# Kernel tuning notes

Hardware: AMD Instinct MI355X
Metric: run time of the kernel (lower is better)

## Reference

```python
import jax, jax.numpy as jnp
import numpy as np

B, N, K = 64, 128, 12
D_ATOM, D_NBR, D_NEW = 256, 320, 256
H, DK = 8, 32  # D_NEW = H * DK
LN_EPS = 1e-5
NEG_INF = -1e9


def setup_inputs() -> dict:
    key = jax.random.key(0)
    ks = jax.random.split(key, 10)
    atom_feature = jax.random.normal(ks[0], (B, N, D_ATOM), jnp.float32)
    atom_neighbor_feature = jax.random.normal(ks[1], (B, N, K, D_NBR), jnp.float32)
    # valid-neighbor masks from random neighbor counts in [1, K]
    counts = jax.random.randint(ks[2], (B, N), 1, K + 1)
    valid = (jnp.arange(K)[None, None, :] < counts[:, :, None]).astype(jnp.float32)
    atom_attend_mask = valid[..., None]                      # (B,N,K,1), 1=real neighbor
    atom_softmax_mask = (1.0 - valid[..., None]) * NEG_INF   # (B,N,K,1), additive
    # parameters
    s = 1.0 / np.sqrt(D_ATOM)
    W_atom = jax.random.uniform(ks[3], (D_ATOM, D_NEW), jnp.float32, -s, s)
    b_atom = jnp.zeros((D_NEW,), jnp.float32)
    s2 = 1.0 / np.sqrt(D_NBR)
    W_nbr = jax.random.uniform(ks[4], (D_NBR, D_NEW), jnp.float32, -s2, s2)
    b_nbr = jnp.zeros((D_NEW,), jnp.float32)
    s3 = 1.0 / np.sqrt(DK)
    w_align = jax.random.uniform(ks[5], (DK, 1), jnp.float32, -s3, s3)
    b_align = jnp.zeros((1,), jnp.float32)
    ln_gamma = jnp.ones((D_NEW,), jnp.float32)
    ln_beta = jnp.zeros((D_NEW,), jnp.float32)
    return dict(atom_feature=atom_feature, atom_neighbor_feature=atom_neighbor_feature,
                atom_softmax_mask=atom_softmax_mask, atom_attend_mask=atom_attend_mask,
                W_atom=W_atom, b_atom=b_atom, W_nbr=W_nbr, b_nbr=b_nbr,
                w_align=w_align, b_align=b_align, ln_gamma=ln_gamma, ln_beta=ln_beta)


def reference(atom_feature, atom_neighbor_feature, atom_softmax_mask, atom_attend_mask,
              W_atom, b_atom, W_nbr, b_nbr, w_align, b_align, ln_gamma, ln_beta):
    # dropout is identity at eval time
    h = atom_feature @ W_atom + b_atom                    # (B,N,D_NEW)
    e = atom_neighbor_feature @ W_nbr + b_nbr             # (B,N,K,D_NEW)
    h = h.reshape(B, N, 1, H, DK)                         # broadcast over K
    e = e.reshape(B, N, K, H, DK)
    # GATv2: act(h_i + e_j) then per-head linear score
    feat = jax.nn.leaky_relu(h + e)                       # slope 0.01 == torch default
    score = feat @ w_align + b_align                      # (B,N,K,H,1)
    score = score + atom_softmax_mask[:, :, :, None, :]   # additive -inf on pad
    attn = jax.nn.softmax(score, axis=2)                  # softmax over neighbors K
    attn = attn * atom_attend_mask[:, :, :, None, :]
    ctx = jnp.sum(attn * e, axis=2).reshape(B, N, H * DK)  # (B,N,D_NEW)
    # LayerNorm
    mu = jnp.mean(ctx, axis=-1, keepdims=True)
    xc = ctx - mu
    var = jnp.mean(xc * xc, axis=-1, keepdims=True)
    return xc * jax.lax.rsqrt(var + LN_EPS) * ln_gamma + ln_beta
```

## Files before the change

kernel.cpp:

```cpp
#include <hip/hip_runtime.h>

#define KN 12
#define DNBR 320
#define DNEW 256
#define BN_TOT 8192
#define ATB 2
#define NKS_E 10
#define NKS_H 8
#define ASTR_E 328
#define ASTR_H 264
#define H_OFF 294912

typedef short bf8_t __attribute__((ext_vector_type(8)));
typedef float f32x4 __attribute__((ext_vector_type(4)));
typedef unsigned short us8 __attribute__((ext_vector_type(8)));
using u16 = unsigned short;
using u32 = unsigned int;

__device__ __forceinline__ u16 f2bf(float f) {
    u32 x = __float_as_uint(f);
    return (u16)((x + 0x7fffu + ((x >> 16) & 1u)) >> 16);
}

__device__ __forceinline__ us8 pack8(float4 a, float4 b) {
    us8 v;
    v[0] = f2bf(a.x); v[1] = f2bf(a.y); v[2] = f2bf(a.z); v[3] = f2bf(a.w);
    v[4] = f2bf(b.x); v[5] = f2bf(b.y); v[6] = f2bf(b.z); v[7] = f2bf(b.w);
    return v;
}

__global__ __launch_bounds__(256) void build_b2(
    const float* __restrict__ Wn, const float* __restrict__ Wa,
    u16* __restrict__ B2)
{
    int tile = blockIdx.x * 4 + (threadIdx.x >> 6);
    int l = threadIdx.x & 63;
    int q = l >> 4, m = l & 15;
    us8 v;
    if (tile < 160) {
        int ks = tile >> 4, nt = tile & 15;
        int col = nt * 16 + m;
#pragma unroll
        for (int e = 0; e < 8; e++)
            v[e] = f2bf(Wn[(ks * 32 + q * 8 + e) * DNEW + col]);
    } else {
        int tt = tile - 160;
        int ks = tt >> 4, nt = tt & 15;
        int col = nt * 16 + m;
#pragma unroll
        for (int e = 0; e < 8; e++)
            v[e] = f2bf(Wa[(ks * 32 + q * 8 + e) * DNEW + col]);
    }
    *(us8*)&B2[(size_t)tile * 512 + l * 8] = v;
}

__global__ __launch_bounds__(256) void h_pre(
    const float* __restrict__ atomf, const u16* __restrict__ B2,
    const float* __restrict__ ba, float* __restrict__ h_g)
{
    __shared__ u16 A[32 * ASTR_H];

    const int t = threadIdx.x;
    const int l = t & 63, w = t >> 6, q = l >> 4, m = l & 15;
    const int ab = blockIdx.x * 32;

    const float* base = atomf + (size_t)ab * DNEW;
    for (int i = t; i < 1024; i += 256) {
        float4 v0 = *(const float4*)(base + i * 8);
        float4 v1 = *(const float4*)(base + i * 8 + 4);
        int a = i >> 5, c8 = i & 31;
        *(us8*)&A[a * ASTR_H + c8 * 8] = pack8(v0, v1);
    }
    __syncthreads();

    f32x4 acc[2][4];
#pragma unroll
    for (int mt = 0; mt < 2; mt++)
#pragma unroll
        for (int j = 0; j < 4; j++) acc[mt][j] = (f32x4){0.f, 0.f, 0.f, 0.f};

    for (int ks = 0; ks < NKS_H; ks++) {
        bf8_t af0 = *(bf8_t*)&A[m * ASTR_H + ks * 32 + q * 8];
        bf8_t af1 = *(bf8_t*)&A[(16 + m) * ASTR_H + ks * 32 + q * 8];
#pragma unroll
        for (int j = 0; j < 4; j++) {
            bf8_t bfj = *(const bf8_t*)&B2[((size_t)(160 + ks * 16 + w * 4 + j) * 64 + l) * 8];
            acc[0][j] = __builtin_amdgcn_mfma_f32_16x16x32_bf16(af0, bfj, acc[0][j], 0, 0, 0);
            acc[1][j] = __builtin_amdgcn_mfma_f32_16x16x32_bf16(af1, bfj, acc[1][j], 0, 0, 0);
        }
    }
#pragma unroll
    for (int mt = 0; mt < 2; mt++)
#pragma unroll
        for (int j = 0; j < 4; j++) {
            int col = w * 64 + j * 16 + m;
            float bav = ba[col];
#pragma unroll
            for (int r = 0; r < 4; r++) {
                int row = ab + mt * 16 + q * 4 + r;
                h_g[(size_t)row * DNEW + col] = acc[mt][j][r] + bav;
            }
        }
}

__global__ __launch_bounds__(256, 6) void fused_all(
    const float* __restrict__ nbrf,
    const float* __restrict__ smaskg, const float* __restrict__ amaskg,
    const u16* __restrict__ B2, const float* __restrict__ h_g,
    const float* __restrict__ bnb, const float* __restrict__ walg,
    const float* __restrict__ balg, const float* __restrict__ gam,
    const float* __restrict__ bet, float* __restrict__ out)
{
    __shared__ u16 A_e[28 * ASTR_E];
    __shared__ float bnb_l[256];
    __shared__ float wal_l[32];
    __shared__ float smask_l[ATB * KN];
    __shared__ float amask_l[ATB * KN];
    __shared__ float red_l[ATB][8];

    const int t = threadIdx.x;
    const int l = t & 63, w = t >> 6, q = l >> 4, m = l & 15;
    const int a0 = blockIdx.x * ATB;

    bnb_l[t] = bnb[t];
    if (t < 32) wal_l[t] = walg[t];
    else if (t >= 32 && t < 32 + ATB * KN)
        smask_l[t - 32] = smaskg[(size_t)a0 * KN + (t - 32)] + balg[0];
    else if (t >= 64 && t < 64 + ATB * KN)
        amask_l[t - 64] = amaskg[(size_t)a0 * KN + (t - 64)];

    const float* nbase = nbrf + (size_t)a0 * (KN * DNBR);
    for (int i = t; i < 960; i += 256) {
        float4 v0 = *(const float4*)(nbase + i * 8);
        float4 v1 = *(const float4*)(nbase + i * 8 + 4);
        int at = i / 480, rem = i - at * 480;
        int row = rem / 40, c8 = rem - row * 40;
        *(us8*)&A_e[(at * 12 + row) * ASTR_E + c8 * 8] = pack8(v0, v1);
    }
    if (t < 164) {
        int rr = t / 41, c8 = t - rr * 41;
        us8 z = {0, 0, 0, 0, 0, 0, 0, 0};
        *(us8*)&A_e[(24 + rr) * ASTR_E + c8 * 8] = z;
    }

    float hv[ATB][4];
#pragma unroll
    for (int j = 0; j < 4; j++) {
        int col = w * 64 + j * 16 + m;
        hv[0][j] = h_g[(size_t)(a0 + 0) * DNEW + col];
        hv[1][j] = h_g[(size_t)(a0 + 1) * DNEW + col];
    }

    __syncthreads();

    f32x4 acc_e[ATB][4];
#pragma unroll
    for (int at = 0; at < ATB; at++)
#pragma unroll
        for (int j = 0; j < 4; j++) acc_e[at][j] = (f32x4){0.f, 0.f, 0.f, 0.f};

    for (int ks = 0; ks < NKS_E; ks++) {
        bf8_t af0 = *(bf8_t*)&A_e[m * ASTR_E + ks * 32 + q * 8];
        bf8_t af1 = *(bf8_t*)&A_e[(12 + m) * ASTR_E + ks * 32 + q * 8];
#pragma unroll
        for (int j = 0; j < 4; j++) {
            bf8_t bfj = *(const bf8_t*)&B2[((size_t)(ks * 16 + w * 4 + j) * 64 + l) * 8];
            acc_e[0][j] = __builtin_amdgcn_mfma_f32_16x16x32_bf16(af0, bfj, acc_e[0][j], 0, 0, 0);
            acc_e[1][j] = __builtin_amdgcn_mfma_f32_16x16x32_bf16(af1, bfj, acc_e[1][j], 0, 0, 0);
        }
    }

#pragma unroll
    for (int j = 0; j < 4; j++) {
        float bv = bnb_l[w * 64 + j * 16 + m];
#pragma unroll
        for (int at = 0; at < ATB; at++)
#pragma unroll
            for (int r = 0; r < 4; r++) acc_e[at][j][r] += bv;
    }

    float wv[4];
#pragma unroll
    for (int j = 0; j < 4; j++) wv[j] = wal_l[(j * 16 + m) & 31];

    float ctxv[ATB][4];
#pragma unroll
    for (int at = 0; at < ATB; at++) {
        float s1 = 0.f, s2 = 0.f;
#pragma unroll
        for (int jj = 0; jj < 2; jj++) {
            float p[4];
#pragma unroll
            for (int r = 0; r < 4; r++) {
                float pp = 0.f;
#pragma unroll
                for (int jo = 0; jo < 2; jo++) {
                    int j = jj * 2 + jo;
                    float f = acc_e[at][j][r] + hv[at][j];
                    f = f > 0.f ? f : 0.01f * f;
                    pp = fmaf(f, wv[j], pp);
                }
                pp += __shfl_xor(pp, 1);
                pp += __shfl_xor(pp, 2);
                pp += __shfl_xor(pp, 4);
                pp += __shfl_xor(pp, 8);
                p[r] = (q < 3) ? pp + smask_l[at * KN + q * 4 + r] : -1e30f;
            }
            float mx = fmaxf(fmaxf(p[0], p[1]), fmaxf(p[2], p[3]));
            mx = fmaxf(mx, __shfl_xor(mx, 16));
            mx = fmaxf(mx, __shfl_xor(mx, 32));
            float ex[4], ss = 0.f;
#pragma unroll
            for (int r = 0; r < 4; r++) {
                ex[r] = (q < 3) ? __expf(p[r] - mx) : 0.f;
                ss += ex[r];
            }
            ss += __shfl_xor(ss, 16);
            ss += __shfl_xor(ss, 32);
            float inv = 1.f / ss;
            float am[4];
#pragma unroll
            for (int r = 0; r < 4; r++)
                am[r] = (q < 3) ? ex[r] * inv * amask_l[at * KN + q * 4 + r] : 0.f;
#pragma unroll
            for (int jo = 0; jo < 2; jo++) {
                int j = jj * 2 + jo;
                float cp = am[0] * acc_e[at][j][0] + am[1] * acc_e[at][j][1] +
                           am[2] * acc_e[at][j][2] + am[3] * acc_e[at][j][3];
                cp += __shfl_xor(cp, 16);
                cp += __shfl_xor(cp, 32);
                ctxv[at][j] = cp;
                s1 += cp;
                s2 += cp * cp;
            }
        }
#pragma unroll
        for (int off = 1; off < 16; off <<= 1) {
            s1 += __shfl_xor(s1, off);
            s2 += __shfl_xor(s2, off);
        }
        if (l == 0) { red_l[at][w] = s1; red_l[at][4 + w] = s2; }
    }
    __syncthreads();

#pragma unroll
    for (int at = 0; at < ATB; at++) {
        float ts1 = red_l[at][0] + red_l[at][1] + red_l[at][2] + red_l[at][3];
        float ts2 = red_l[at][4] + red_l[at][5] + red_l[at][6] + red_l[at][7];
        float mu = ts1 * (1.f / 256.f);
        float var = ts2 * (1.f / 256.f) - mu * mu;
        var = fmaxf(var, 0.f);
        float rs = rsqrtf(var + 1e-5f);
        if (q == 0) {
#pragma unroll
            for (int j = 0; j < 4; j++) {
                int col = w * 64 + j * 16 + m;
                out[(size_t)(a0 + at) * DNEW + col] =
                    (ctxv[at][j] - mu) * rs * gam[col] + bet[col];
            }
        }
    }
}

extern "C" void kernel_launch(void* const* d_in, const int* in_sizes, int n_in,
                              void* d_out, int out_size, void* d_ws, size_t ws_size,
                              hipStream_t stream) {
    const float* atomf = (const float*)d_in[0];
    const float* nbrf  = (const float*)d_in[1];
    const float* smask = (const float*)d_in[2];
    const float* amask = (const float*)d_in[3];
    const float* Wa    = (const float*)d_in[4];
    const float* ba    = (const float*)d_in[5];
    const float* Wn    = (const float*)d_in[6];
    const float* bnb   = (const float*)d_in[7];
    const float* wal   = (const float*)d_in[8];
    const float* bal   = (const float*)d_in[9];
    const float* gam   = (const float*)d_in[10];
    const float* bet   = (const float*)d_in[11];
    float* outp = (float*)d_out;

    u16* B2 = (u16*)d_ws;
    float* h_g = (float*)((char*)d_ws + H_OFF);

    build_b2<<<72, 256, 0, stream>>>(Wn, Wa, B2);
    h_pre<<<BN_TOT / 32, 256, 0, stream>>>(atomf, B2, ba, h_g);
    fused_all<<<BN_TOT / ATB, 256, 0, stream>>>(nbrf, smask, amask, B2, h_g,
                                                bnb, wal, bal, gam, bet, outp);
}
```

Baseline: 265.3 us.

## Load neighbor features directly into MFMA A-fragments, dropping LDS staging

The neighbor-feature tile no longer goes through shared memory. Each lane now loads its own fp32 neighbor row slice from global memory and converts it to bf16 in registers with v_cvt_pk_bf16_f32. Bias, align weights and masks are read straight into registers, which removes the LDS buffer and the __syncthreads. Each of the four waves in a block now reloads the same A data from global memory (leaning on the cache), and the occupancy hint drops from 6 to 4 blocks to leave more register room.

Result: slower. 289.2 us (+9.0%).

```diff
diff --git a/kernel.cpp b/kernel.cpp
--- a/kernel.cpp
+++ b/kernel.cpp
@@ -7,7 +7,6 @@
 #define ATB 2
 #define NKS_E 10
 #define NKS_H 8
-#define ASTR_E 328
 #define ASTR_H 264
 #define H_OFF 294912
 
@@ -27,6 +26,17 @@
     v[0] = f2bf(a.x); v[1] = f2bf(a.y); v[2] = f2bf(a.z); v[3] = f2bf(a.w);
     v[4] = f2bf(b.x); v[5] = f2bf(b.y); v[6] = f2bf(b.z); v[7] = f2bf(b.w);
     return v;
+}
+
+__device__ __forceinline__ bf8_t cvt8(float4 a, float4 b) {
+    u32 r0, r1, r2, r3;
+    asm("v_cvt_pk_bf16_f32 %0, %1, %2" : "=v"(r0) : "v"(a.x), "v"(a.y));
+    asm("v_cvt_pk_bf16_f32 %0, %1, %2" : "=v"(r1) : "v"(a.z), "v"(a.w));
+    asm("v_cvt_pk_bf16_f32 %0, %1, %2" : "=v"(r2) : "v"(b.x), "v"(b.y));
+    asm("v_cvt_pk_bf16_f32 %0, %1, %2" : "=v"(r3) : "v"(b.z), "v"(b.w));
+    union { u32 u[4]; bf8_t v; } cv;
+    cv.u[0] = r0; cv.u[1] = r1; cv.u[2] = r2; cv.u[3] = r3;
+    return cv.v;
 }
 
 __global__ __launch_bounds__(256) void build_b2(
@@ -103,7 +113,7 @@
         }
 }
 
-__global__ __launch_bounds__(256, 6) void fused_all(
+__global__ __launch_bounds__(256, 4) void fused_all(
     const float* __restrict__ nbrf,
     const float* __restrict__ smaskg, const float* __restrict__ amaskg,
     const u16* __restrict__ B2, const float* __restrict__ h_g,
@@ -111,47 +121,37 @@
     const float* __restrict__ balg, const float* __restrict__ gam,
     const float* __restrict__ bet, float* __restrict__ out)
 {
-    __shared__ u16 A_e[28 * ASTR_E];
-    __shared__ float bnb_l[256];
-    __shared__ float wal_l[32];
-    __shared__ float smask_l[ATB * KN];
-    __shared__ float amask_l[ATB * KN];
     __shared__ float red_l[ATB][8];
 
     const int t = threadIdx.x;
     const int l = t & 63, w = t >> 6, q = l >> 4, m = l & 15;
     const int a0 = blockIdx.x * ATB;
 
-    bnb_l[t] = bnb[t];
-    if (t < 32) wal_l[t] = walg[t];
-    else if (t >= 32 && t < 32 + ATB * KN)
-        smask_l[t - 32] = smaskg[(size_t)a0 * KN + (t - 32)] + balg[0];
-    else if (t >= 64 && t < 64 + ATB * KN)
-        amask_l[t - 64] = amaskg[(size_t)a0 * KN + (t - 64)];
-
-    const float* nbase = nbrf + (size_t)a0 * (KN * DNBR);
-    for (int i = t; i < 960; i += 256) {
-        float4 v0 = *(const float4*)(nbase + i * 8);
-        float4 v1 = *(const float4*)(nbase + i * 8 + 4);
-        int at = i / 480, rem = i - at * 480;
-        int row = rem / 40, c8 = rem - row * 40;
-        *(us8*)&A_e[(at * 12 + row) * ASTR_E + c8 * 8] = pack8(v0, v1);
-    }
-    if (t < 164) {
-        int rr = t / 41, c8 = t - rr * 41;
-        us8 z = {0, 0, 0, 0, 0, 0, 0, 0};
-        *(us8*)&A_e[(24 + rr) * ASTR_E + c8 * 8] = z;
-    }
-
-    float hv[ATB][4];
+    const float bal = balg[0];
+    float hv[ATB][4], bnbv[4], wv[4];
 #pragma unroll
     for (int j = 0; j < 4; j++) {
         int col = w * 64 + j * 16 + m;
         hv[0][j] = h_g[(size_t)(a0 + 0) * DNEW + col];
         hv[1][j] = h_g[(size_t)(a0 + 1) * DNEW + col];
-    }
-
-    __syncthreads();
+        bnbv[j] = bnb[col];
+        wv[j] = walg[(j * 16 + m) & 31];
+    }
+    const bool qv = (q < 3);
+    float smv[ATB][4], amv[ATB][4];
+#pragma unroll
+    for (int at = 0; at < ATB; at++)
+#pragma unroll
+        for (int r = 0; r < 4; r++) {
+            int k = q * 4 + r;
+            smv[at][r] = qv ? smaskg[(size_t)(a0 + at) * KN + k] + bal : 0.f;
+            amv[at][r] = qv ? amaskg[(size_t)(a0 + at) * KN + k] : 0.f;
+        }
+
+    const bool mval = (m < KN);
+    const float* ab0 = nbrf + ((size_t)(a0 + 0) * KN + m) * DNBR;
+    const float* ab1 = nbrf + ((size_t)(a0 + 1) * KN + m) * DNBR;
+    const int ko = q * 8;
 
     f32x4 acc_e[ATB][4];
 #pragma unroll
@@ -159,9 +159,16 @@
 #pragma unroll
         for (int j = 0; j < 4; j++) acc_e[at][j] = (f32x4){0.f, 0.f, 0.f, 0.f};
 
+#pragma unroll
     for (int ks = 0; ks < NKS_E; ks++) {
-        bf8_t af0 = *(bf8_t*)&A_e[m * ASTR_E + ks * 32 + q * 8];
-        bf8_t af1 = *(bf8_t*)&A_e[(12 + m) * ASTR_E + ks * 32 + q * 8];
+        bf8_t af0 = (bf8_t){0, 0, 0, 0, 0, 0, 0, 0};
+        bf8_t af1 = (bf8_t){0, 0, 0, 0, 0, 0, 0, 0};
+        if (mval) {
+            const float* p0 = ab0 + ks * 32 + ko;
+            const float* p1 = ab1 + ks * 32 + ko;
+            af0 = cvt8(*(const float4*)p0, *(const float4*)(p0 + 4));
+            af1 = cvt8(*(const float4*)p1, *(const float4*)(p1 + 4));
+        }
 #pragma unroll
         for (int j = 0; j < 4; j++) {
             bf8_t bfj = *(const bf8_t*)&B2[((size_t)(ks * 16 + w * 4 + j) * 64 + l) * 8];
@@ -172,16 +179,11 @@
 
 #pragma unroll
     for (int j = 0; j < 4; j++) {
-        float bv = bnb_l[w * 64 + j * 16 + m];
 #pragma unroll
         for (int at = 0; at < ATB; at++)
 #pragma unroll
-            for (int r = 0; r < 4; r++) acc_e[at][j][r] += bv;
-    }
-
-    float wv[4];
-#pragma unroll
-    for (int j = 0; j < 4; j++) wv[j] = wal_l[(j * 16 + m) & 31];
+            for (int r = 0; r < 4; r++) acc_e[at][j][r] += bnbv[j];
+    }
 
     float ctxv[ATB][4];
 #pragma unroll
@@ -204,7 +206,7 @@
                 pp += __shfl_xor(pp, 2);
                 pp += __shfl_xor(pp, 4);
                 pp += __shfl_xor(pp, 8);
-                p[r] = (q < 3) ? pp + smask_l[at * KN + q * 4 + r] : -1e30f;
+                p[r] = qv ? pp + smv[at][r] : -1e30f;
             }
             float mx = fmaxf(fmaxf(p[0], p[1]), fmaxf(p[2], p[3]));
             mx = fmaxf(mx, __shfl_xor(mx, 16));
@@ -212,7 +214,7 @@
             float ex[4], ss = 0.f;
 #pragma unroll
             for (int r = 0; r < 4; r++) {
-                ex[r] = (q < 3) ? __expf(p[r] - mx) : 0.f;
+                ex[r] = qv ? __expf(p[r] - mx) : 0.f;
                 ss += ex[r];
             }
             ss += __shfl_xor(ss, 16);
@@ -221,7 +223,7 @@
             float am[4];
 #pragma unroll
             for (int r = 0; r < 4; r++)
-                am[r] = (q < 3) ? ex[r] * inv * amask_l[at * KN + q * 4 + r] : 0.f;
+                am[r] = qv ? ex[r] * inv * amv[at][r] : 0.f;
 #pragma unroll
             for (int jo = 0; jo < 2; jo++) {
                 int j = jj * 2 + jo;
```
